# Optimization experiments

Measured on AMD Instinct MI355X. Metric: run time of the kernel, lower is better.

## Reference

```python
import jax, jax.numpy as jnp
import numpy as np

N = 100000
D_IN = 64
D_HID = 64


def _sage_conv(x, edge_index, Wl, bl, Wr):
    # PyG SAGEConv (mean aggr): out = lin_l(mean_j x_j) + lin_r(x_root)
    src, dst = edge_index[0], edge_index[1]
    n = x.shape[0]
    msg_sum = jax.ops.segment_sum(x[src], dst, num_segments=n)  # [N, d]
    deg = jax.ops.segment_sum(jnp.ones_like(src, dtype=x.dtype), dst, num_segments=n)
    agg = msg_sum / jnp.maximum(deg, 1.0)[:, None]
    return agg @ Wl + bl + x @ Wr


def setup_inputs() -> dict:
    key = jax.random.key(0)
    ks = jax.random.split(key, 8)
    x = jax.random.normal(ks[0], (N, D_IN), dtype=jnp.float32)
    edge_index = jax.random.randint(ks[1], (2, 16 * N), 0, N, dtype=jnp.int64)
    s = 1.0 / np.sqrt(D_IN)
    W1l = jax.random.uniform(ks[2], (D_IN, D_HID), minval=-s, maxval=s, dtype=jnp.float32)
    b1 = jnp.zeros((D_HID,), dtype=jnp.float32)
    W1r = jax.random.uniform(ks[3], (D_IN, D_HID), minval=-s, maxval=s, dtype=jnp.float32)
    s2 = 1.0 / np.sqrt(D_HID)
    W2l = jax.random.uniform(ks[4], (D_HID, D_HID), minval=-s2, maxval=s2, dtype=jnp.float32)
    b2 = jnp.zeros((D_HID,), dtype=jnp.float32)
    W2r = jax.random.uniform(ks[5], (D_HID, D_HID), minval=-s2, maxval=s2, dtype=jnp.float32)
    Wc = jax.random.uniform(ks[6], (D_HID, 2), minval=-s2, maxval=s2, dtype=jnp.float32)
    bc = jax.random.uniform(ks[7], (2,), minval=-s2, maxval=s2, dtype=jnp.float32)
    return {"x": x, "edge_index": edge_index, "W1l": W1l, "b1": b1, "W1r": W1r,
            "W2l": W2l, "b2": b2, "W2r": W2r, "Wc": Wc, "bc": bc}


def reference(x, edge_index, W1l, b1, W1r, W2l, b2, W2r, Wc, bc):
    h = jax.nn.relu(_sage_conv(x, edge_index, W1l, b1, W1r))
    h = _sage_conv(h, edge_index, W2l, b2, W2r)
    return h @ Wc + bc  # [N, 2] logits
```

## Files before the change

kernel.cpp:

```cpp
#include <hip/hip_runtime.h>


#define SCAN_BS 1024
#define BUCKET_BITS 8
#define BUCKET_NODES 256
#define NBUCK_MAX 512
#define EPB 2048
#define STAGE_CAP 5120

__global__ void __launch_bounds__(256) bucket_hist_kernel(const int* __restrict__ dst,
                                                          int* __restrict__ counts,
                                                          int ne, int B, int NB) {
  __shared__ int hist[NBUCK_MAX];
  for (int k = threadIdx.x; k < B; k += 256) hist[k] = 0;
  __syncthreads();
  int base = blockIdx.x * EPB;
#pragma unroll 4
  for (int i = 0; i < EPB / 256; ++i) {
    int e = base + i * 256 + threadIdx.x;
    if (e < ne) atomicAdd(&hist[dst[e] >> BUCKET_BITS], 1);
  }
  __syncthreads();
  for (int k = threadIdx.x; k < B; k += 256) counts[k * NB + blockIdx.x] = hist[k];
}

__device__ __forceinline__ int block_scan_inclusive_1024(int v, int* wsums) {
  int lane = threadIdx.x & 63;
  int wid = threadIdx.x >> 6;
  int s = v;
#pragma unroll
  for (int off = 1; off < 64; off <<= 1) {
    int t = __shfl_up(s, off);
    if (lane >= off) s += t;
  }
  if (lane == 63) wsums[wid] = s;
  __syncthreads();
  if (wid == 0) {
    int ws = (lane < 16) ? wsums[lane] : 0;
#pragma unroll
    for (int off = 1; off < 16; off <<= 1) {
      int t = __shfl_up(ws, off);
      if (lane >= off) ws += t;
    }
    if (lane < 16) wsums[lane] = ws;
  }
  __syncthreads();
  if (wid > 0) s += wsums[wid - 1];
  return s;
}

__device__ __forceinline__ int block_scan_inclusive_256(int v, int* wsums4) {
  int lane = threadIdx.x & 63;
  int wid = threadIdx.x >> 6;
  int s = v;
#pragma unroll
  for (int off = 1; off < 64; off <<= 1) {
    int t = __shfl_up(s, off);
    if (lane >= off) s += t;
  }
  if (lane == 63) wsums4[wid] = s;
  __syncthreads();
  if (wid == 0) {
    int ws = (lane < 4) ? wsums4[lane] : 0;
#pragma unroll
    for (int off = 1; off < 4; off <<= 1) {
      int t = __shfl_up(ws, off);
      if (lane >= off) ws += t;
    }
    if (lane < 4) wsums4[lane] = ws;
  }
  __syncthreads();
  if (wid > 0) s += wsums4[wid - 1];
  return s;
}

__global__ void __launch_bounds__(SCAN_BS) scan_a_inplace_kernel(int* __restrict__ data,
                                                                 int* __restrict__ bsums,
                                                                 int S) {
  __shared__ int wsums[16];
  int i = blockIdx.x * SCAN_BS + threadIdx.x;
  int v = (i < S) ? data[i] : 0;
  int inc = block_scan_inclusive_1024(v, wsums);
  if (i < S) data[i] = inc - v;
  if (threadIdx.x == SCAN_BS - 1) bsums[blockIdx.x] = inc;
}

__global__ void __launch_bounds__(SCAN_BS) scan_b_kernel(const int* __restrict__ bsums,
                                                         int* __restrict__ boffs, int nb) {
  __shared__ int wsums[16];
  int v = ((int)threadIdx.x < nb) ? bsums[threadIdx.x] : 0;
  int inc = block_scan_inclusive_1024(v, wsums);
  if ((int)threadIdx.x < nb) boffs[threadIdx.x] = inc - v;
  if ((int)threadIdx.x == nb - 1) boffs[nb] = inc;
}

__global__ void __launch_bounds__(256) bucket_place_kernel(const int* __restrict__ src,
                                                           const int* __restrict__ dst,
                                                           const int* __restrict__ counts,
                                                           const int* __restrict__ boffs,
                                                           int* __restrict__ arr,
                                                           int ne, int B, int NB) {
  __shared__ int cur[NBUCK_MAX];
  for (int k = threadIdx.x; k < B; k += 256) {
    int idx = k * NB + blockIdx.x;
    cur[k] = counts[idx] + boffs[idx >> 10];
  }
  __syncthreads();
  int base = blockIdx.x * EPB;
#pragma unroll 4
  for (int i = 0; i < EPB / 256; ++i) {
    int e = base + i * 256 + threadIdx.x;
    if (e < ne) {
      int d = dst[e];
      int k = d >> BUCKET_BITS;
      int pos = atomicAdd(&cur[k], 1);
      arr[pos] = (src[e] << BUCKET_BITS) | (d & (BUCKET_NODES - 1));
    }
  }
}

__global__ void __launch_bounds__(256) csr_bucket_kernel(const int* __restrict__ arr,
                                                         const int* __restrict__ counts,
                                                         const int* __restrict__ boffs,
                                                         int* __restrict__ row_ptr,
                                                         int* __restrict__ col,
                                                         int n, int ne, int B, int NB) {
  __shared__ int hist[BUCKET_NODES];
  __shared__ int cur[BUCKET_NODES];
  __shared__ int stage[STAGE_CAP];
  __shared__ int wsums4[4];
  int k = blockIdx.x;
  int tid = threadIdx.x;
  int i0 = k * NB;
  int start = counts[i0] + boffs[i0 >> 10];
  int end;
  if (k + 1 < B) {
    int i1 = (k + 1) * NB;
    end = counts[i1] + boffs[i1 >> 10];
  } else {
    end = ne;
  }
  int size = end - start;
  hist[tid] = 0;
  __syncthreads();
  for (int e = start + tid; e < end; e += 256)
    atomicAdd(&hist[arr[e] & (BUCKET_NODES - 1)], 1);
  __syncthreads();
  int v = hist[tid];
  int inc = block_scan_inclusive_256(v, wsums4);
  int e0 = inc - v;
  cur[tid] = e0;
  {
    int node = k * BUCKET_NODES + tid;
    if (node < n) row_ptr[node] = start + e0;
  }
  if (k == B - 1 && tid == 0) row_ptr[n] = ne;
  __syncthreads();
  for (int e = start + tid; e < end; e += 256) {
    int p = arr[e];
    int pos = atomicAdd(&cur[p & (BUCKET_NODES - 1)], 1);
    int s = p >> BUCKET_BITS;
    if (pos < STAGE_CAP) stage[pos] = s;
    else col[start + pos] = s;
  }
  __syncthreads();
  int lim = (size < STAGE_CAP) ? size : STAGE_CAP;
  for (int i = tid; i < lim; i += 256) col[start + i] = stage[i];
}

__global__ void __launch_bounds__(256) aggregate_kernel(const float* __restrict__ xin,
                                                        const int* __restrict__ row_ptr,
                                                        const int* __restrict__ col,
                                                        float* __restrict__ outp, int n) {
  int gwave = (blockIdx.x * 256 + threadIdx.x) >> 6;
  int lane = threadIdx.x & 63;
  if (gwave >= n) return;
  int m = __builtin_amdgcn_readfirstlane(gwave);
  int start = row_ptr[m];
  int end = row_ptr[m + 1];
  float a[16];
#pragma unroll
  for (int i = 0; i < 16; ++i) a[i] = 0.f;
  int e = start;
  for (; e + 16 <= end; e += 16) {
    int c[16];
#pragma unroll
    for (int i = 0; i < 16; ++i) c[i] = col[e + i];
#pragma unroll
    for (int i = 0; i < 16; ++i) a[i] += xin[(size_t)c[i] * 64 + lane];
  }
  for (; e + 4 <= end; e += 4) {
    int c0 = col[e + 0], c1 = col[e + 1], c2 = col[e + 2], c3 = col[e + 3];
    a[0] += xin[(size_t)c0 * 64 + lane];
    a[1] += xin[(size_t)c1 * 64 + lane];
    a[2] += xin[(size_t)c2 * 64 + lane];
    a[3] += xin[(size_t)c3 * 64 + lane];
  }
  for (; e < end; ++e) a[0] += xin[(size_t)col[e] * 64 + lane];
#pragma unroll
  for (int i = 8; i > 0; i >>= 1)
#pragma unroll
    for (int j = 0; j < i; ++j) a[j] += a[j + i];
  int d = end - start;
  float inv = 1.0f / (float)((d > 0) ? d : 1);
  outp[(size_t)m * 64 + lane] = a[0] * inv;
}

#define GBM 128

__device__ __forceinline__ void gemm_phase(const float* __restrict__ M,
                                           const float* __restrict__ W,
                                           float (&Mt)[GBM][65], float (&Ws)[64][64],
                                           float4 (&acc)[8],
                                           int node0, int n, int tx, int ty, int t) {
  __syncthreads();
#pragma unroll
  for (int i = 0; i < 8; ++i) {
    int f4 = i * 256 + t;
    int r = f4 >> 4, c4 = f4 & 15;
    int nd = node0 + r;
    float4 v = make_float4(0.f, 0.f, 0.f, 0.f);
    if (nd < n) v = ((const float4*)(M + (size_t)nd * 64))[c4];
    Mt[r][c4 * 4 + 0] = v.x; Mt[r][c4 * 4 + 1] = v.y;
    Mt[r][c4 * 4 + 2] = v.z; Mt[r][c4 * 4 + 3] = v.w;
  }
#pragma unroll
  for (int i = 0; i < 4; ++i) {
    int f4 = i * 256 + t;
    int k = f4 >> 4, c4 = f4 & 15;
    float4 v = ((const float4*)W)[f4];
    *(float4*)&Ws[k][c4 * 4] = v;
  }
  __syncthreads();
#pragma unroll 4
  for (int k = 0; k < 64; ++k) {
    float4 w4 = *(const float4*)&Ws[k][tx * 4];
    float a[8];
#pragma unroll
    for (int m = 0; m < 8; ++m) a[m] = Mt[ty * 8 + m][k];
#pragma unroll
    for (int m = 0; m < 8; ++m) {
      acc[m].x = fmaf(a[m], w4.x, acc[m].x);
      acc[m].y = fmaf(a[m], w4.y, acc[m].y);
      acc[m].z = fmaf(a[m], w4.z, acc[m].z);
      acc[m].w = fmaf(a[m], w4.w, acc[m].w);
    }
  }
}

__global__ void __launch_bounds__(256) gemm_relu_kernel(const float* __restrict__ A,
                                                        const float* __restrict__ X,
                                                        const float* __restrict__ Wl,
                                                        const float* __restrict__ bias,
                                                        const float* __restrict__ Wr,
                                                        float* __restrict__ H, int n) {
  __shared__ float Mt[GBM][65];
  __shared__ float Ws[64][64];
  int t = threadIdx.x;
  int tx = t & 15, ty = t >> 4;
  int node0 = blockIdx.x * GBM;
  float4 bv = *(const float4*)(bias + tx * 4);
  float4 acc[8];
#pragma unroll
  for (int m = 0; m < 8; ++m) acc[m] = bv;
  gemm_phase(A, Wl, Mt, Ws, acc, node0, n, tx, ty, t);
  gemm_phase(X, Wr, Mt, Ws, acc, node0, n, tx, ty, t);
#pragma unroll
  for (int m = 0; m < 8; ++m) {
    int nd = node0 + ty * 8 + m;
    if (nd < n) {
      float4 v;
      v.x = fmaxf(acc[m].x, 0.f);
      v.y = fmaxf(acc[m].y, 0.f);
      v.z = fmaxf(acc[m].z, 0.f);
      v.w = fmaxf(acc[m].w, 0.f);
      ((float4*)(H + (size_t)nd * 64))[tx] = v;
    }
  }
}

__global__ void __launch_bounds__(256) gemm_cls_kernel(const float* __restrict__ A,
                                                       const float* __restrict__ X,
                                                       const float* __restrict__ Wl,
                                                       const float* __restrict__ bias,
                                                       const float* __restrict__ Wr,
                                                       const float* __restrict__ Wc,
                                                       const float* __restrict__ bc,
                                                       float* __restrict__ outp, int n) {
  __shared__ float Mt[GBM][65];
  __shared__ float Ws[64][64];
  int t = threadIdx.x;
  int tx = t & 15, ty = t >> 4;
  int node0 = blockIdx.x * GBM;
  float4 bv = *(const float4*)(bias + tx * 4);
  float4 acc[8];
#pragma unroll
  for (int m = 0; m < 8; ++m) acc[m] = bv;
  gemm_phase(A, Wl, Mt, Ws, acc, node0, n, tx, ty, t);
  gemm_phase(X, Wr, Mt, Ws, acc, node0, n, tx, ty, t);
  float2 wc0 = *(const float2*)(Wc + (tx * 4 + 0) * 2);
  float2 wc1 = *(const float2*)(Wc + (tx * 4 + 1) * 2);
  float2 wc2 = *(const float2*)(Wc + (tx * 4 + 2) * 2);
  float2 wc3 = *(const float2*)(Wc + (tx * 4 + 3) * 2);
  float b0 = bc[0], b1 = bc[1];
#pragma unroll
  for (int m = 0; m < 8; ++m) {
    float p0 = acc[m].x * wc0.x + acc[m].y * wc1.x + acc[m].z * wc2.x + acc[m].w * wc3.x;
    float p1 = acc[m].x * wc0.y + acc[m].y * wc1.y + acc[m].z * wc2.y + acc[m].w * wc3.y;
#pragma unroll
    for (int off = 1; off < 16; off <<= 1) {
      p0 += __shfl_xor(p0, off);
      p1 += __shfl_xor(p1, off);
    }
    if (tx == 0) {
      int nd = node0 + ty * 8 + m;
      if (nd < n) {
        float2 o;
        o.x = p0 + b0;
        o.y = p1 + b1;
        *(float2*)(outp + (size_t)nd * 2) = o;
      }
    }
  }
}

extern "C" void kernel_launch(void* const* d_in, const int* in_sizes, int n_in,
                              void* d_out, int out_size, void* d_ws, size_t ws_size,
                              hipStream_t stream) {
  const float* x   = (const float*)d_in[0];
  const int*   ei  = (const int*)d_in[1];
  const float* W1l = (const float*)d_in[2];
  const float* b1  = (const float*)d_in[3];
  const float* W1r = (const float*)d_in[4];
  const float* W2l = (const float*)d_in[5];
  const float* b2  = (const float*)d_in[6];
  const float* W2r = (const float*)d_in[7];
  const float* Wc  = (const float*)d_in[8];
  const float* bc  = (const float*)d_in[9];
  float* out = (float*)d_out;

  const int n  = in_sizes[0] / 64;
  const int ne = in_sizes[1] / 2;
  const int* src = ei;
  const int* dst = ei + ne;

  const int B  = (n + BUCKET_NODES - 1) >> BUCKET_BITS;
  const int NB = (ne + EPB - 1) / EPB;
  const int S  = B * NB;
  const int nsb = (S + SCAN_BS - 1) / SCAN_BS;

  char* ws = (char*)d_ws;
  size_t off = 0;
  auto carve = [&](size_t bytes) -> void* {
    void* p = ws + off;
    off += (bytes + 255) & ~(size_t)255;
    return p;
  };
  int* counts  = (int*)carve((size_t)S * 4);
  int* bsums   = (int*)carve((size_t)(nsb + 1) * 4);
  int* boffs   = (int*)carve((size_t)(nsb + 1) * 4);
  int* col     = (int*)carve((size_t)ne * 4);
  int* row_ptr = (int*)carve((size_t)(n + 1) * 4);
  float* m1    = (float*)carve((size_t)n * 64 * 4);
  float* h     = (float*)carve((size_t)n * 64 * 4);
  int* arr     = (int*)m1;
  (void)ws_size;

  bucket_hist_kernel<<<NB, 256, 0, stream>>>(dst, counts, ne, B, NB);
  scan_a_inplace_kernel<<<nsb, SCAN_BS, 0, stream>>>(counts, bsums, S);
  scan_b_kernel<<<1, SCAN_BS, 0, stream>>>(bsums, boffs, nsb);
  bucket_place_kernel<<<NB, 256, 0, stream>>>(src, dst, counts, boffs, arr, ne, B, NB);
  csr_bucket_kernel<<<B, 256, 0, stream>>>(arr, counts, boffs, row_ptr, col, n, ne, B, NB);

  const int gtiles = (n + GBM - 1) / GBM;
  aggregate_kernel<<<(n * 64 + 255) / 256, 256, 0, stream>>>(x, row_ptr, col, m1, n);
  gemm_relu_kernel<<<gtiles, 256, 0, stream>>>(m1, x, W1l, b1, W1r, h, n);

  aggregate_kernel<<<(n * 64 + 255) / 256, 256, 0, stream>>>(h, row_ptr, col, m1, n);
  gemm_cls_kernel<<<gtiles, 256, 0, stream>>>(m1, h, W2l, b2, W2r, Wc, bc, out, n);
}
```

Measured before the change: 316.5 us.

## Fuse CSR-build kernels into one cooperative kernel with grid syncs

Replaces the five CSR-construction kernels (bucket histogram, two-level scan, bucket placement, per-bucket sort) with a single cooperative kernel that separates the phases with grid.sync. The 1024-thread scan is done with 256 threads handling four elements each. The aim is to remove kernel launch gaps and tail effects between the small build phases. In exchange it adds grid-wide barriers and requires all NB blocks (about 782) to be co-resident, with larger shared memory per block that may limit occupancy.

```diff
diff --git a/kernel.cpp b/kernel.cpp
--- a/kernel.cpp
+++ b/kernel.cpp
@@ -1,55 +1,17 @@
 #include <hip/hip_runtime.h>
-
-
-#define SCAN_BS 1024
+#include <hip/hip_cooperative_groups.h>
+
+namespace cg = cooperative_groups;
+
+
 #define BUCKET_BITS 8
 #define BUCKET_NODES 256
 #define NBUCK_MAX 512
 #define EPB 2048
 #define STAGE_CAP 5120
-
-__global__ void __launch_bounds__(256) bucket_hist_kernel(const int* __restrict__ dst,
-                                                          int* __restrict__ counts,
-                                                          int ne, int B, int NB) {
-  __shared__ int hist[NBUCK_MAX];
-  for (int k = threadIdx.x; k < B; k += 256) hist[k] = 0;
-  __syncthreads();
-  int base = blockIdx.x * EPB;
-#pragma unroll 4
-  for (int i = 0; i < EPB / 256; ++i) {
-    int e = base + i * 256 + threadIdx.x;
-    if (e < ne) atomicAdd(&hist[dst[e] >> BUCKET_BITS], 1);
-  }
-  __syncthreads();
-  for (int k = threadIdx.x; k < B; k += 256) counts[k * NB + blockIdx.x] = hist[k];
-}
-
-__device__ __forceinline__ int block_scan_inclusive_1024(int v, int* wsums) {
-  int lane = threadIdx.x & 63;
-  int wid = threadIdx.x >> 6;
-  int s = v;
-#pragma unroll
-  for (int off = 1; off < 64; off <<= 1) {
-    int t = __shfl_up(s, off);
-    if (lane >= off) s += t;
-  }
-  if (lane == 63) wsums[wid] = s;
-  __syncthreads();
-  if (wid == 0) {
-    int ws = (lane < 16) ? wsums[lane] : 0;
-#pragma unroll
-    for (int off = 1; off < 16; off <<= 1) {
-      int t = __shfl_up(ws, off);
-      if (lane >= off) ws += t;
-    }
-    if (lane < 16) wsums[lane] = ws;
-  }
-  __syncthreads();
-  if (wid > 0) s += wsums[wid - 1];
-  return s;
-}
-
-__device__ __forceinline__ int block_scan_inclusive_256(int v, int* wsums4) {
+#define SMEM_INTS 5636
+
+__device__ __forceinline__ int scan256(int v, int* wsums4) {
   int lane = threadIdx.x & 63;
   int wid = threadIdx.x >> 6;
   int s = v;
@@ -74,98 +36,128 @@
   return s;
 }
 
-__global__ void __launch_bounds__(SCAN_BS) scan_a_inplace_kernel(int* __restrict__ data,
-                                                                 int* __restrict__ bsums,
-                                                                 int S) {
-  __shared__ int wsums[16];
-  int i = blockIdx.x * SCAN_BS + threadIdx.x;
-  int v = (i < S) ? data[i] : 0;
-  int inc = block_scan_inclusive_1024(v, wsums);
-  if (i < S) data[i] = inc - v;
-  if (threadIdx.x == SCAN_BS - 1) bsums[blockIdx.x] = inc;
-}
-
-__global__ void __launch_bounds__(SCAN_BS) scan_b_kernel(const int* __restrict__ bsums,
-                                                         int* __restrict__ boffs, int nb) {
-  __shared__ int wsums[16];
-  int v = ((int)threadIdx.x < nb) ? bsums[threadIdx.x] : 0;
-  int inc = block_scan_inclusive_1024(v, wsums);
-  if ((int)threadIdx.x < nb) boffs[threadIdx.x] = inc - v;
-  if ((int)threadIdx.x == nb - 1) boffs[nb] = inc;
-}
-
-__global__ void __launch_bounds__(256) bucket_place_kernel(const int* __restrict__ src,
-                                                           const int* __restrict__ dst,
-                                                           const int* __restrict__ counts,
-                                                           const int* __restrict__ boffs,
-                                                           int* __restrict__ arr,
-                                                           int ne, int B, int NB) {
-  __shared__ int cur[NBUCK_MAX];
-  for (int k = threadIdx.x; k < B; k += 256) {
-    int idx = k * NB + blockIdx.x;
-    cur[k] = counts[idx] + boffs[idx >> 10];
-  }
-  __syncthreads();
-  int base = blockIdx.x * EPB;
+__global__ void __launch_bounds__(256) build_coop_kernel(
+    const int* __restrict__ src, const int* __restrict__ dst,
+    int* __restrict__ counts, int* __restrict__ bsums, int* __restrict__ boffs,
+    int* __restrict__ arr, int* __restrict__ row_ptr, int* __restrict__ col,
+    int n, int ne, int B, int NB, int S, int nsb) {
+  cg::grid_group grid = cg::this_grid();
+  __shared__ int smem[SMEM_INTS];
+  int* wsums4 = smem + SMEM_INTS - 4;
+  int tid = threadIdx.x;
+  int b = blockIdx.x;
+
+  if (b < NB) {
+    int* hist = smem;
+    for (int k = tid; k < B; k += 256) hist[k] = 0;
+    __syncthreads();
+    int base = b * EPB;
 #pragma unroll 4
-  for (int i = 0; i < EPB / 256; ++i) {
-    int e = base + i * 256 + threadIdx.x;
-    if (e < ne) {
-      int d = dst[e];
-      int k = d >> BUCKET_BITS;
-      int pos = atomicAdd(&cur[k], 1);
-      arr[pos] = (src[e] << BUCKET_BITS) | (d & (BUCKET_NODES - 1));
-    }
-  }
-}
-
-__global__ void __launch_bounds__(256) csr_bucket_kernel(const int* __restrict__ arr,
-                                                         const int* __restrict__ counts,
-                                                         const int* __restrict__ boffs,
-                                                         int* __restrict__ row_ptr,
-                                                         int* __restrict__ col,
-                                                         int n, int ne, int B, int NB) {
-  __shared__ int hist[BUCKET_NODES];
-  __shared__ int cur[BUCKET_NODES];
-  __shared__ int stage[STAGE_CAP];
-  __shared__ int wsums4[4];
-  int k = blockIdx.x;
-  int tid = threadIdx.x;
-  int i0 = k * NB;
-  int start = counts[i0] + boffs[i0 >> 10];
-  int end;
-  if (k + 1 < B) {
-    int i1 = (k + 1) * NB;
-    end = counts[i1] + boffs[i1 >> 10];
-  } else {
-    end = ne;
-  }
-  int size = end - start;
-  hist[tid] = 0;
-  __syncthreads();
-  for (int e = start + tid; e < end; e += 256)
-    atomicAdd(&hist[arr[e] & (BUCKET_NODES - 1)], 1);
-  __syncthreads();
-  int v = hist[tid];
-  int inc = block_scan_inclusive_256(v, wsums4);
-  int e0 = inc - v;
-  cur[tid] = e0;
-  {
-    int node = k * BUCKET_NODES + tid;
-    if (node < n) row_ptr[node] = start + e0;
-  }
-  if (k == B - 1 && tid == 0) row_ptr[n] = ne;
-  __syncthreads();
-  for (int e = start + tid; e < end; e += 256) {
-    int p = arr[e];
-    int pos = atomicAdd(&cur[p & (BUCKET_NODES - 1)], 1);
-    int s = p >> BUCKET_BITS;
-    if (pos < STAGE_CAP) stage[pos] = s;
-    else col[start + pos] = s;
-  }
-  __syncthreads();
-  int lim = (size < STAGE_CAP) ? size : STAGE_CAP;
-  for (int i = tid; i < lim; i += 256) col[start + i] = stage[i];
+    for (int i = 0; i < EPB / 256; ++i) {
+      int e = base + i * 256 + tid;
+      if (e < ne) atomicAdd(&hist[dst[e] >> BUCKET_BITS], 1);
+    }
+    __syncthreads();
+    for (int k = tid; k < B; k += 256) counts[k * NB + b] = hist[k];
+  }
+  __threadfence();
+  grid.sync();
+
+  if (b < nsb) {
+    int i0 = b * 1024 + tid * 4;
+    int v0 = (i0 + 0 < S) ? counts[i0 + 0] : 0;
+    int v1 = (i0 + 1 < S) ? counts[i0 + 1] : 0;
+    int v2 = (i0 + 2 < S) ? counts[i0 + 2] : 0;
+    int v3 = (i0 + 3 < S) ? counts[i0 + 3] : 0;
+    int ts = v0 + v1 + v2 + v3;
+    int inc = scan256(ts, wsums4);
+    int e0 = inc - ts;
+    if (i0 + 0 < S) counts[i0 + 0] = e0;
+    if (i0 + 1 < S) counts[i0 + 1] = e0 + v0;
+    if (i0 + 2 < S) counts[i0 + 2] = e0 + v0 + v1;
+    if (i0 + 3 < S) counts[i0 + 3] = e0 + v0 + v1 + v2;
+    if (tid == 255) bsums[b] = inc;
+  }
+  __threadfence();
+  grid.sync();
+
+  if (b == 0) {
+    int j0 = tid * 2, j1 = tid * 2 + 1;
+    int v0 = (j0 < nsb) ? bsums[j0] : 0;
+    int v1 = (j1 < nsb) ? bsums[j1] : 0;
+    int ts = v0 + v1;
+    int inc = scan256(ts, wsums4);
+    int e0 = inc - ts;
+    if (j0 < nsb) boffs[j0] = e0;
+    if (j1 < nsb) boffs[j1] = e0 + v0;
+    if (tid == 255) boffs[nsb] = inc;
+  }
+  __threadfence();
+  grid.sync();
+
+  if (b < NB) {
+    int* cur = smem;
+    for (int k = tid; k < B; k += 256) {
+      int idx = k * NB + b;
+      cur[k] = counts[idx] + boffs[idx >> 10];
+    }
+    __syncthreads();
+    int base = b * EPB;
+#pragma unroll 4
+    for (int i = 0; i < EPB / 256; ++i) {
+      int e = base + i * 256 + tid;
+      if (e < ne) {
+        int d = dst[e];
+        int k = d >> BUCKET_BITS;
+        int pos = atomicAdd(&cur[k], 1);
+        arr[pos] = (src[e] << BUCKET_BITS) | (d & (BUCKET_NODES - 1));
+      }
+    }
+  }
+  __threadfence();
+  grid.sync();
+
+  if (b < B) {
+    int* histc = smem;
+    int* curc  = smem + 256;
+    int* stage = smem + 512;
+    int k = b;
+    int i0 = k * NB;
+    int start = counts[i0] + boffs[i0 >> 10];
+    int end;
+    if (k + 1 < B) {
+      int i1 = (k + 1) * NB;
+      end = counts[i1] + boffs[i1 >> 10];
+    } else {
+      end = ne;
+    }
+    int size = end - start;
+    histc[tid] = 0;
+    __syncthreads();
+    for (int e = start + tid; e < end; e += 256)
+      atomicAdd(&histc[arr[e] & (BUCKET_NODES - 1)], 1);
+    __syncthreads();
+    int v = histc[tid];
+    int inc = scan256(v, wsums4);
+    int e0 = inc - v;
+    curc[tid] = e0;
+    {
+      int node = k * BUCKET_NODES + tid;
+      if (node < n) row_ptr[node] = start + e0;
+    }
+    if (k == B - 1 && tid == 0) row_ptr[n] = ne;
+    __syncthreads();
+    for (int e = start + tid; e < end; e += 256) {
+      int p = arr[e];
+      int pos = atomicAdd(&curc[p & (BUCKET_NODES - 1)], 1);
+      int s = p >> BUCKET_BITS;
+      if (pos < STAGE_CAP) stage[pos] = s;
+      else col[start + pos] = s;
+    }
+    __syncthreads();
+    int lim = (size < STAGE_CAP) ? size : STAGE_CAP;
+    for (int i = tid; i < lim; i += 256) col[start + i] = stage[i];
+  }
 }
 
 __global__ void __launch_bounds__(256) aggregate_kernel(const float* __restrict__ xin,
@@ -339,15 +331,15 @@
   const float* bc  = (const float*)d_in[9];
   float* out = (float*)d_out;
 
-  const int n  = in_sizes[0] / 64;
-  const int ne = in_sizes[1] / 2;
+  int n  = in_sizes[0] / 64;
+  int ne = in_sizes[1] / 2;
   const int* src = ei;
   const int* dst = ei + ne;
 
-  const int B  = (n + BUCKET_NODES - 1) >> BUCKET_BITS;
-  const int NB = (ne + EPB - 1) / EPB;
-  const int S  = B * NB;
-  const int nsb = (S + SCAN_BS - 1) / SCAN_BS;
+  int B   = (n + BUCKET_NODES - 1) >> BUCKET_BITS;
+  int NB  = (ne + EPB - 1) / EPB;
+  int S   = B * NB;
+  int nsb = (S + 1023) / 1024;
 
   char* ws = (char*)d_ws;
   size_t off = 0;
@@ -366,11 +358,16 @@
   int* arr     = (int*)m1;
   (void)ws_size;
 
-  bucket_hist_kernel<<<NB, 256, 0, stream>>>(dst, counts, ne, B, NB);
-  scan_a_inplace_kernel<<<nsb, SCAN_BS, 0, stream>>>(counts, bsums, S);
-  scan_b_kernel<<<1, SCAN_BS, 0, stream>>>(bsums, boffs, nsb);
-  bucket_place_kernel<<<NB, 256, 0, stream>>>(src, dst, counts, boffs, arr, ne, B, NB);
-  csr_bucket_kernel<<<B, 256, 0, stream>>>(arr, counts, boffs, row_ptr, col, n, ne, B, NB);
+  {
+    const int* src_ = src;
+    const int* dst_ = dst;
+    void* args[] = {(void*)&src_, (void*)&dst_, (void*)&counts, (void*)&bsums,
+                    (void*)&boffs, (void*)&arr, (void*)&row_ptr, (void*)&col,
+                    (void*)&n, (void*)&ne, (void*)&B, (void*)&NB,
+                    (void*)&S, (void*)&nsb};
+    hipLaunchCooperativeKernel((void*)build_coop_kernel, dim3(NB), dim3(256),
+                               args, 0, stream);
+  }
 
   const int gtiles = (n + GBM - 1) / GBM;
   aggregate_kernel<<<(n * 64 + 255) / 256, 256, 0, stream>>>(x, row_ptr, col, m1, n);
```

Measured after the change: 966.5 us. +205.4%, slower.
